# Kernel optimization log

Hardware: AMD Instinct MI355X
Metric: run time of the kernel (lower is better)

## Reference

```python
import jax, jax.numpy as jnp
import numpy as np

C = 1.0          # ball curvature (c in MidpointMLR)
B = 1048576      # batch
F_IN = 64        # num_features
F_OUT = 64       # num_classes
EPS = 1e-15


def setup_inputs() -> dict:
    key = jax.random.key(0)
    k1, k2, k3 = jax.random.split(key, 3)
    # points well inside the Poincare ball
    x = 0.05 * jax.random.normal(k1, (B, F_IN), dtype=jnp.float32)
    # PoincareLinear params: z [in, out], bias [out]
    z = jax.random.normal(k2, (F_IN, F_OUT), dtype=jnp.float32) * (1.0 / np.sqrt(F_IN))
    bias = 0.01 * jax.random.normal(k3, (F_OUT,), dtype=jnp.float32)
    return {"x": x, "z": z, "bias": bias}


def reference(x, z, bias):
    """HNN++ PoincareLinear: unidirectional Poincare MLR + map back into the ball."""
    c = jnp.float32(C)
    rc = jnp.sqrt(c)
    # split z into direction and magnitude (column-wise)
    z_norm = jnp.maximum(jnp.linalg.norm(z, axis=0), EPS)   # [out]
    z_unit = z / z_norm                                      # [in, out]
    # unidirectional Poincare MLR logits
    rcx = rc * x                                             # [B, in]
    cx2 = jnp.sum(rcx * rcx, axis=-1, keepdims=True)         # [B, 1] = c*||x||^2
    drcr = 2.0 * rc * bias                                   # [out]
    num = 2.0 * (rcx @ z_unit) * jnp.cosh(drcr) - (1.0 + cx2) * jnp.sinh(drcr)
    logits = (2.0 * z_norm / rc) * jnp.arcsinh(num / jnp.maximum(1.0 - cx2, EPS))  # [B, out]
    # map distances back onto the ball: x -> sinh(rc*x)/rc, then gyro-projection
    y = jnp.sinh(rc * logits) / rc
    return y / (1.0 + jnp.sqrt(1.0 + c * jnp.sum(y * y, axis=-1, keepdims=True)))
```

## Files before the change

kernel.cpp:

```cpp
#include <hip/hip_runtime.h>
#include <math.h>


#define MLR_B 1048576

typedef __bf16 bf16x8 __attribute__((ext_vector_type(8)));
typedef float  f32x4  __attribute__((ext_vector_type(4)));

__global__ __launch_bounds__(256) void mlr_prep_kernel(const float* __restrict__ z,
                                                       const float* __restrict__ bias,
                                                       void* __restrict__ wsv) {
    __bf16* zf   = (__bf16*)wsv;
    f32x4*  cst4 = (f32x4*)((char*)wsv + 8192);
    __shared__ float part[4][64];
    __shared__ float invs[64];

    const int tid = threadIdx.x;
    const int o   = tid & 63;
    const int kq  = tid >> 6;

    float n2 = 0.f;
#pragma unroll
    for (int kk = 0; kk < 16; ++kk) {
        int k = kq * 16 + kk;
        float v = z[k * 64 + o];
        n2 = fmaf(v, v, n2);
    }
    part[kq][o] = n2;
    __syncthreads();

    if (tid < 64) {
        float tot = part[0][o] + part[1][o] + part[2][o] + part[3][o];
        float zn  = fmaxf(sqrtf(tot), 1e-15f);
        invs[o] = 1.f / zn;
        float d = 2.f * bias[o];
        cst4[o] = (f32x4){2.f * coshf(d), sinhf(d), 2.f * zn, 0.f};
    }
    __syncthreads();

    const float inv = invs[o];
    const int t = o & 3, c = o >> 2;
#pragma unroll
    for (int kk = 0; kk < 16; ++kk) {
        int k  = kq * 16 + kk;
        float zu = z[k * 64 + o] * inv;
        int i  = k >> 4;
        int j  = k & 3;
        int hi = (k >> 2) & 3;
        int s  = i >> 1;
        int e  = ((i & 1) << 2) | j;
        zf[(s * 4 + t) * 512 + (hi * 16 + c) * 8 + e] = (__bf16)zu;
    }
}

__device__ __forceinline__ float poin_y(float dot, float ch2, float sh, float g,
                                        float opc, float rden) {
    float t = fmaf(dot, ch2, -(opc * sh)) * rden;
    float a = fabsf(t);
    float u = a + sqrtf(fmaf(a, a, 1.f));
    float w = __builtin_amdgcn_exp2f(g * __builtin_amdgcn_logf(u));
    float y = 0.5f * (w - __builtin_amdgcn_rcpf(w));
    return copysignf(y, t);
}

__device__ __forceinline__ void mlr_step(f32x4 c0, f32x4 c1, f32x4 c2, f32x4 c3,
                                         const bf16x8* bfr, const f32x4* cc,
                                         int lo, int hi, char* ob) {
    float p = 0.f;
#pragma unroll
    for (int j = 0; j < 4; ++j) {
        p = fmaf(c0[j], c0[j], p); p = fmaf(c1[j], c1[j], p);
        p = fmaf(c2[j], c2[j], p); p = fmaf(c3[j], c3[j], p);
    }
    p += __shfl_xor(p, 16);
    p += __shfl_xor(p, 32);

    bf16x8 a0, a1;
#pragma unroll
    for (int j = 0; j < 4; ++j) {
        a0[j]     = (__bf16)c0[j];
        a0[4 + j] = (__bf16)c1[j];
        a1[j]     = (__bf16)c2[j];
        a1[4 + j] = (__bf16)c3[j];
    }

    f32x4 acc[4];
#pragma unroll
    for (int t = 0; t < 4; ++t) {
        acc[t] = (f32x4){0.f, 0.f, 0.f, 0.f};
        acc[t] = __builtin_amdgcn_mfma_f32_16x16x32_bf16(a0, bfr[t],     acc[t], 0, 0, 0);
        acc[t] = __builtin_amdgcn_mfma_f32_16x16x32_bf16(a1, bfr[4 + t], acc[t], 0, 0, 0);
    }

    f32x4 yv[4]; float S[4];
#pragma unroll
    for (int r = 0; r < 4; ++r) {
        float cxr  = __shfl(p, hi * 4 + r);
        float opc  = 1.f + cxr;
        float rden = __builtin_amdgcn_rcpf(fmaxf(1.f - cxr, 1e-15f));
        float s0 = 0.f;
        f32x4 y;
#pragma unroll
        for (int t = 0; t < 4; ++t) {
            float v = poin_y(acc[t][r], cc[t].x, cc[t].y, cc[t].z, opc, rden);
            y[t] = v;
            s0 = fmaf(v, v, s0);
        }
        yv[r] = y;
        S[r] = s0;
    }
#pragma unroll
    for (int r = 0; r < 4; ++r) {
        float s0 = S[r];
        s0 += __shfl_xor(s0, 1);
        s0 += __shfl_xor(s0, 2);
        s0 += __shfl_xor(s0, 4);
        s0 += __shfl_xor(s0, 8);
        float scale = __builtin_amdgcn_rcpf(1.f + sqrtf(1.f + s0));
        f32x4 y = yv[r];
        y[0] *= scale; y[1] *= scale; y[2] *= scale; y[3] *= scale;
        yv[r] = y;
    }

#pragma unroll
    for (int r = 0; r < 4; ++r)
        __builtin_nontemporal_store(yv[r], (f32x4*)(ob + r * 256));
}

__global__ __launch_bounds__(256) void mlr_main_kernel(const float* __restrict__ x,
                                                       const void* __restrict__ wsv,
                                                       float* __restrict__ out) {
    const __bf16* zf   = (const __bf16*)wsv;
    const f32x4*  cst4 = (const f32x4*)((const char*)wsv + 8192);
    const int tid  = threadIdx.x;
    const int lane = tid & 63;
    const int lo   = lane & 15;
    const int hi   = lane >> 4;
    const int wv   = blockIdx.x * 4 + (tid >> 6);

    bf16x8 bfr[8];
#pragma unroll
    for (int i = 0; i < 8; ++i)
        bfr[i] = *(const bf16x8*)((const char*)zf + i * 1024 + lane * 16);
    f32x4 cc[4];
#pragma unroll
    for (int t = 0; t < 4; ++t) cc[t] = cst4[4 * lo + t];

    const size_t rowbase = (size_t)wv * 32;
    const char* xb = (const char*)x + (rowbase + (size_t)lo) * 256 + hi * 16;

    f32x4 c0 = __builtin_nontemporal_load((const f32x4*)(xb + 0));
    f32x4 c1 = __builtin_nontemporal_load((const f32x4*)(xb + 64));
    f32x4 c2 = __builtin_nontemporal_load((const f32x4*)(xb + 128));
    f32x4 c3 = __builtin_nontemporal_load((const f32x4*)(xb + 192));
    f32x4 d0 = __builtin_nontemporal_load((const f32x4*)(xb + 4096 + 0));
    f32x4 d1 = __builtin_nontemporal_load((const f32x4*)(xb + 4096 + 64));
    f32x4 d2 = __builtin_nontemporal_load((const f32x4*)(xb + 4096 + 128));
    f32x4 d3 = __builtin_nontemporal_load((const f32x4*)(xb + 4096 + 192));

    char* ob = (char*)out + (rowbase + (size_t)hi * 4) * 256 + lo * 16;
    mlr_step(c0, c1, c2, c3, bfr, cc, lo, hi, ob);
    mlr_step(d0, d1, d2, d3, bfr, cc, lo, hi, ob + 4096);
}

extern "C" void kernel_launch(void* const* d_in, const int* in_sizes, int n_in,
                              void* d_out, int out_size, void* d_ws, size_t ws_size,
                              hipStream_t stream) {
    const float* x    = (const float*)d_in[0];
    const float* z    = (const float*)d_in[1];
    const float* bias = (const float*)d_in[2];
    float* out = (float*)d_out;

    mlr_prep_kernel<<<dim3(1), dim3(256), 0, stream>>>(z, bias, d_ws);
    mlr_main_kernel<<<dim3(8192), dim3(256), 0, stream>>>(x, d_ws, out);
}
```

Measured before the change: 112.5 us.

## Split MLR step into gemm and finish, interleave second tile load

Splits the per-tile step into a GEMM phase and an epilogue phase. The second tile's loads are now issued after the first GEMM and overlap with the first epilogue. It also swaps the nontemporal loads for plain loads, adds a min-blocks-per-SM launch bound, and drops the abs/copysign handling in the arcsinh/sinh path. The sign simplification relies on the identity sinh(g*asinh(t)) being odd, but it uses t+sqrt(t^2+1), which loses precision for negative t through cancellation.

Result: faster. 96.62 us (-14.1%).

```diff
diff --git a/kernel.cpp b/kernel.cpp
--- a/kernel.cpp
+++ b/kernel.cpp
@@ -56,16 +56,19 @@
 __device__ __forceinline__ float poin_y(float dot, float ch2, float sh, float g,
                                         float opc, float rden) {
     float t = fmaf(dot, ch2, -(opc * sh)) * rden;
-    float a = fabsf(t);
-    float u = a + sqrtf(fmaf(a, a, 1.f));
+    float u = t + sqrtf(fmaf(t, t, 1.f));
     float w = __builtin_amdgcn_exp2f(g * __builtin_amdgcn_logf(u));
-    float y = 0.5f * (w - __builtin_amdgcn_rcpf(w));
-    return copysignf(y, t);
+    return 0.5f * (w - __builtin_amdgcn_rcpf(w));
 }
 
-__device__ __forceinline__ void mlr_step(f32x4 c0, f32x4 c1, f32x4 c2, f32x4 c3,
-                                         const bf16x8* bfr, const f32x4* cc,
-                                         int lo, int hi, char* ob) {
+struct StepMid {
+    f32x4 acc[4];
+    float p;
+};
+
+__device__ __forceinline__ StepMid mlr_gemm(f32x4 c0, f32x4 c1, f32x4 c2, f32x4 c3,
+                                            const bf16x8* bfr) {
+    StepMid m;
     float p = 0.f;
 #pragma unroll
     for (int j = 0; j < 4; ++j) {
@@ -74,6 +77,7 @@
     }
     p += __shfl_xor(p, 16);
     p += __shfl_xor(p, 32);
+    m.p = p;
 
     bf16x8 a0, a1;
 #pragma unroll
@@ -84,25 +88,28 @@
         a1[4 + j] = (__bf16)c3[j];
     }
 
-    f32x4 acc[4];
 #pragma unroll
     for (int t = 0; t < 4; ++t) {
-        acc[t] = (f32x4){0.f, 0.f, 0.f, 0.f};
-        acc[t] = __builtin_amdgcn_mfma_f32_16x16x32_bf16(a0, bfr[t],     acc[t], 0, 0, 0);
-        acc[t] = __builtin_amdgcn_mfma_f32_16x16x32_bf16(a1, bfr[4 + t], acc[t], 0, 0, 0);
+        m.acc[t] = (f32x4){0.f, 0.f, 0.f, 0.f};
+        m.acc[t] = __builtin_amdgcn_mfma_f32_16x16x32_bf16(a0, bfr[t],     m.acc[t], 0, 0, 0);
+        m.acc[t] = __builtin_amdgcn_mfma_f32_16x16x32_bf16(a1, bfr[4 + t], m.acc[t], 0, 0, 0);
     }
+    return m;
+}
 
+__device__ __forceinline__ void mlr_fin(const StepMid& m, const f32x4* cc,
+                                        int lo, int hi, char* ob) {
     f32x4 yv[4]; float S[4];
 #pragma unroll
     for (int r = 0; r < 4; ++r) {
-        float cxr  = __shfl(p, hi * 4 + r);
+        float cxr  = __shfl(m.p, hi * 4 + r);
         float opc  = 1.f + cxr;
         float rden = __builtin_amdgcn_rcpf(fmaxf(1.f - cxr, 1e-15f));
         float s0 = 0.f;
         f32x4 y;
 #pragma unroll
         for (int t = 0; t < 4; ++t) {
-            float v = poin_y(acc[t][r], cc[t].x, cc[t].y, cc[t].z, opc, rden);
+            float v = poin_y(m.acc[t][r], cc[t].x, cc[t].y, cc[t].z, opc, rden);
             y[t] = v;
             s0 = fmaf(v, v, s0);
         }
@@ -121,15 +128,14 @@
         y[0] *= scale; y[1] *= scale; y[2] *= scale; y[3] *= scale;
         yv[r] = y;
     }
-
 #pragma unroll
     for (int r = 0; r < 4; ++r)
         __builtin_nontemporal_store(yv[r], (f32x4*)(ob + r * 256));
 }
 
-__global__ __launch_bounds__(256) void mlr_main_kernel(const float* __restrict__ x,
-                                                       const void* __restrict__ wsv,
-                                                       float* __restrict__ out) {
+__global__ __launch_bounds__(256, 4) void mlr_main_kernel(const float* __restrict__ x,
+                                                          const void* __restrict__ wsv,
+                                                          float* __restrict__ out) {
     const __bf16* zf   = (const __bf16*)wsv;
     const f32x4*  cst4 = (const f32x4*)((const char*)wsv + 8192);
     const int tid  = threadIdx.x;
@@ -148,19 +154,24 @@
 
     const size_t rowbase = (size_t)wv * 32;
     const char* xb = (const char*)x + (rowbase + (size_t)lo) * 256 + hi * 16;
+    char* ob = (char*)out + (rowbase + (size_t)hi * 4) * 256 + lo * 16;
 
-    f32x4 c0 = __builtin_nontemporal_load((const f32x4*)(xb + 0));
-    f32x4 c1 = __builtin_nontemporal_load((const f32x4*)(xb + 64));
-    f32x4 c2 = __builtin_nontemporal_load((const f32x4*)(xb + 128));
-    f32x4 c3 = __builtin_nontemporal_load((const f32x4*)(xb + 192));
-    f32x4 d0 = __builtin_nontemporal_load((const f32x4*)(xb + 4096 + 0));
-    f32x4 d1 = __builtin_nontemporal_load((const f32x4*)(xb + 4096 + 64));
-    f32x4 d2 = __builtin_nontemporal_load((const f32x4*)(xb + 4096 + 128));
-    f32x4 d3 = __builtin_nontemporal_load((const f32x4*)(xb + 4096 + 192));
+    f32x4 c0 = *(const f32x4*)(xb + 0);
+    f32x4 c1 = *(const f32x4*)(xb + 64);
+    f32x4 c2 = *(const f32x4*)(xb + 128);
+    f32x4 c3 = *(const f32x4*)(xb + 192);
 
-    char* ob = (char*)out + (rowbase + (size_t)hi * 4) * 256 + lo * 16;
-    mlr_step(c0, c1, c2, c3, bfr, cc, lo, hi, ob);
-    mlr_step(d0, d1, d2, d3, bfr, cc, lo, hi, ob + 4096);
+    StepMid m0 = mlr_gemm(c0, c1, c2, c3, bfr);
+
+    f32x4 d0 = *(const f32x4*)(xb + 4096 + 0);
+    f32x4 d1 = *(const f32x4*)(xb + 4096 + 64);
+    f32x4 d2 = *(const f32x4*)(xb + 4096 + 128);
+    f32x4 d3 = *(const f32x4*)(xb + 4096 + 192);
+
+    mlr_fin(m0, cc, lo, hi, ob);
+
+    StepMid m1 = mlr_gemm(d0, d1, d2, d3, bfr);
+    mlr_fin(m1, cc, lo, hi, ob + 4096);
 }
 
 extern "C" void kernel_launch(void* const* d_in, const int* in_sizes, int n_in,
```
